# Performance work log

Measured on AMD Instinct MI355X. Metric: run time of the kernel, lower is better.

The kernel has to match this reference:

```python
import jax, jax.numpy as jnp
import numpy as np
from jax import lax

B, T, D, H = 4, 2048, 1024, 8
DK = D // H        # head qk dim (expand_k=1.0) = 128
DV = 2 * D // H    # head v dim (expand_v=2.0) = 256
C = 64             # retention chunk size


def setup_inputs() -> dict:
    key = jax.random.key(0)
    ks = jax.random.split(key, 7)
    s = 0.02
    return {
        "x": jax.random.normal(ks[0], (B, T, D), jnp.float32),
        "Wq": jax.random.normal(ks[1], (D, H * DK), jnp.float32) * s,
        "Wk": jax.random.normal(ks[2], (D, H * DK), jnp.float32) * s,
        "Wv": jax.random.normal(ks[3], (D, H * DV), jnp.float32) * s,
        "Wg": jax.random.normal(ks[4], (D, H * DV), jnp.float32) * s,
        "Wo": jax.random.normal(ks[5], (H * DV, D), jnp.float32) * s,
        "norm_w": jnp.ones((DV,), jnp.float32),
    }


def _rope(x):
    # x: [B,T,H,DK]; GPT-NeoX style (non-interleaved) rotary, base 10000
    half = DK // 2
    inv = 1.0 / (10000.0 ** (jnp.arange(0, DK, 2, dtype=jnp.float32) / DK))
    f = jnp.arange(T, dtype=jnp.float32)[:, None] * inv[None, :]  # [T, half]
    cos = jnp.cos(f)[None, :, None, :]
    sin = jnp.sin(f)[None, :, None, :]
    x1, x2 = x[..., :half], x[..., half:]
    return jnp.concatenate([x1 * cos - x2 * sin, x2 * cos + x1 * sin], axis=-1)


def _retention(q, k, v):
    # chunked decay-gated linear attention (RetNet retention)
    # q,k: [B,T,H,DK], v: [B,T,H,DV]; recurrence S_t = g*S_{t-1} + k_t^T v_t, o_t = q_t S_t
    N = T // C
    gamma = 1.0 - 2.0 ** (-5.0 - jnp.arange(H, dtype=jnp.float32))  # [H] per-head decay
    i = jnp.arange(C, dtype=jnp.float32)
    expo = i[:, None] - i[None, :]                                   # [C,C]
    M = jnp.where(expo >= 0, gamma[:, None, None] ** expo[None], 0.0)  # [H,C,C] intra-chunk decay mask
    dec_q = gamma[:, None] ** (i + 1.0)        # [H,C] decay of state seen by q_i
    dec_k = gamma[:, None] ** (C - 1.0 - i)    # [H,C] decay of k_j into end-of-chunk state
    gC = gamma ** C

    def to_chunks(t):
        return t.reshape(B, N, C, H, -1).transpose(1, 0, 3, 2, 4)  # [N,B,H,C,d]

    qs, kcs, vcs = to_chunks(q), to_chunks(k), to_chunks(v)

    def step(S, inp):
        qc, kc, vc = inp  # [B,H,C,DK],[B,H,C,DK],[B,H,C,DV]
        attn = jnp.einsum('bhid,bhjd->bhij', qc, kc) * M[None]
        o_intra = jnp.einsum('bhij,bhje->bhie', attn, vc)
        o_inter = jnp.einsum('bhid,bhde->bhie', qc, S) * dec_q[None, :, :, None]
        kv = jnp.einsum('bhjd,bhje->bhde', kc * dec_k[None, :, :, None], vc)
        S_new = gC[None, :, None, None] * S + kv
        return S_new, o_intra + o_inter

    S0 = jnp.zeros((B, H, DK, DV), q.dtype)
    _, os_ = lax.scan(step, S0, (qs, kcs, vcs))  # os_: [N,B,H,C,DV]
    return os_.transpose(1, 0, 3, 2, 4).reshape(B, T, H, DV)


def reference(x, Wq, Wk, Wv, Wg, Wo, norm_w):
    q = (x @ Wq).reshape(B, T, H, DK)
    k = (x @ Wk).reshape(B, T, H, DK)
    v = (x @ Wv).reshape(B, T, H, DV)
    g = (x @ Wg).reshape(B, T, H, DV)
    q, k = _rope(q), _rope(k)
    q = q * (DK ** -0.5)
    o = _retention(q, k, v)
    # fused per-head RMSNorm + swish output gate (FusedRMSNormSwishGate)
    rms = jnp.sqrt(jnp.mean(o * o, axis=-1, keepdims=True) + 1e-5)
    o = (o / rms) * norm_w
    o = o * g * jax.nn.sigmoid(g)
    return o.reshape(B, T, H * DV) @ Wo
```

## Files before the change

kernel.cpp:

```cpp
#include <hip/hip_runtime.h>
#include <hip/hip_bf16.h>
#include <cstdint>
#include <cstddef>

using f32x4 = __attribute__((ext_vector_type(4))) float;
using s16x8 = __attribute__((ext_vector_type(8))) short;
using s16x4 = __attribute__((ext_vector_type(4))) short;

#define DEVINL __device__ __forceinline__

static constexpr int T_LEN  = 2048;
static constexpr int MROWS  = 8192;
static constexpr int NCHUNK = 32;

DEVINL float bf2f(short s){
  unsigned u = ((unsigned)(unsigned short)s) << 16;
  return __builtin_bit_cast(float, u);
}
DEVINL short f2bf(float f){
  unsigned u = __builtin_bit_cast(unsigned, f);
  u = (u + 0x7fffu + ((u >> 16) & 1u)) >> 16;
  return (short)(unsigned short)u;
}

#define GLOAD16(gp, lp) \
  __builtin_amdgcn_global_load_lds((__attribute__((address_space(1))) void*)(gp), \
                                   (__attribute__((address_space(3))) void*)(lp), 16, 0, 0)

#define MFMA16(a, b, c) __builtin_amdgcn_mfma_f32_16x16x32_bf16((a), (b), (c), 0, 0, 0)
#define SBAR()  __builtin_amdgcn_sched_barrier(0)
#define WAITVM(n)   asm volatile("s_waitcnt vmcnt(" #n ")" ::: "memory")

__global__ __launch_bounds__(256) void cvt_f32_bf16(const float* __restrict__ in,
                                                    short* __restrict__ out, int n4){
  int i = blockIdx.x * 256 + threadIdx.x;
  if (i >= n4) return;
  float4 v = ((const float4*)in)[i];
  short4 o;
  o.x = f2bf(v.x); o.y = f2bf(v.y); o.z = f2bf(v.z); o.w = f2bf(v.w);
  ((short4*)out)[i] = o;
}

__global__ __launch_bounds__(256) void tr_w(const float* __restrict__ in,
                                            short* __restrict__ out, int R, int C){
  __shared__ float tile[32][33];
  int c0 = blockIdx.x * 32, r0 = blockIdx.y * 32;
  int tx = threadIdx.x, ty = threadIdx.y;
  #pragma unroll
  for (int i = 0; i < 4; ++i){
    int r = ty + i * 8;
    tile[r][tx] = in[(size_t)(r0 + r) * C + c0 + tx];
  }
  __syncthreads();
  #pragma unroll
  for (int i = 0; i < 4; ++i){
    int c = ty + i * 8;
    out[(size_t)(c0 + c) * R + r0 + tx] = f2bf(tile[tx][c]);
  }
}

__global__ __launch_bounds__(256) void tr_w4(const float* __restrict__ Wq,
                                             const float* __restrict__ Wk,
                                             const float* __restrict__ Wv,
                                             const float* __restrict__ Wg,
                                             short* __restrict__ WT){
  __shared__ float tile[32][33];
  int bx = blockIdx.x;
  const float* src; int C; size_t off; int cb;
  if (bx < 32)       { src = Wq; C = 1024; off = 0;                       cb = bx; }
  else if (bx < 64)  { src = Wk; C = 1024; off = (size_t)1024 * 1024;     cb = bx - 32; }
  else if (bx < 128) { src = Wg; C = 2048; off = (size_t)2048 * 1024;     cb = bx - 64; }
  else               { src = Wv; C = 2048; off = (size_t)4096 * 1024;     cb = bx - 128; }
  int c0 = cb * 32, r0 = blockIdx.y * 32;
  int tx = threadIdx.x, ty = threadIdx.y;
  #pragma unroll
  for (int i = 0; i < 4; ++i){
    int r = ty + i * 8;
    tile[r][tx] = src[(size_t)(r0 + r) * C + c0 + tx];
  }
  __syncthreads();
  #pragma unroll
  for (int i = 0; i < 4; ++i){
    int c = ty + i * 8;
    WT[off + (size_t)(c0 + c) * 1024 + r0 + tx] = f2bf(tile[tx][c]);
  }
}

__global__ __launch_bounds__(256) void rope_table(float* __restrict__ tab){
  int i = blockIdx.x * 256 + threadIdx.x;
  int t = i >> 6, d = i & 63;
  float inv = exp2f(-(float)d * (13.287712379549449f / 64.0f));
  float f = (float)t * inv;
  float s, c;
  sincosf(f, &s, &c);
  tab[2 * i]     = c;
  tab[2 * i + 1] = s;
}

__global__ __launch_bounds__(256) void rope_q(short* __restrict__ qb,
                                              const float* __restrict__ tab){
  int idx = blockIdx.x * 256 + threadIdx.x;
  int bt  = idx >> 9, rem = idx & 511;
  int h   = rem >> 6, d = rem & 63;
  int t   = bt & (T_LEN - 1);
  float2 cs = ((const float2*)tab)[t * 64 + d];
  float lg = log2f(1.0f - exp2f(-(float)(5 + h)));
  float mult = 0.08838834764831845f * exp2f((float)((t & 63) + 1) * lg);
  size_t base = (size_t)bt * 1024 + h * 128 + d;
  float x1 = bf2f(qb[base]), x2 = bf2f(qb[base + 64]);
  qb[base]      = f2bf((x1 * cs.x - x2 * cs.y) * mult);
  qb[base + 64] = f2bf((x2 * cs.x + x1 * cs.y) * mult);
}

__global__ __launch_bounds__(256) void rope_k_tr(short* __restrict__ kb,
                                                 short* __restrict__ kTt,
                                                 const float* __restrict__ tab){
  __shared__ alignas(16) short T[64 * 128];
  __shared__ alignas(16) short U[128 * 68];
  const int tid = threadIdx.x, wave = tid >> 6, lane = tid & 63;
  const int bt0 = blockIdx.x * 64, h = blockIdx.y;
  const float lg = log2f(1.0f - exp2f(-(float)(5 + h)));
  #pragma unroll
  for (int c = 0; c < 4; ++c){
    int rbase = c * 16 + wave * 4;
    GLOAD16(kb + (size_t)(bt0 + rbase + (lane >> 4)) * 1024 + h * 128 + (lane & 15) * 8,
            T + rbase * 128);
  }
  WAITVM(0);
  __syncthreads();
  {
    int r = tid >> 2, dbase = (tid & 3) * 16;
    int t = (bt0 + r) & (T_LEN - 1);
    float dec = exp2f((float)(63 - r) * lg);
    s16x8 lo[2], hi[2];
    #pragma unroll
    for (int i = 0; i < 16; ++i){
      int d = dbase + i;
      float2 cs = ((const float2*)tab)[t * 64 + d];
      float x1 = bf2f(T[r * 128 + d]);
      float x2 = bf2f(T[r * 128 + 64 + d]);
      float y1 = x1 * cs.x - x2 * cs.y;
      float y2 = x2 * cs.x + x1 * cs.y;
      lo[i >> 3][i & 7] = f2bf(y1);
      hi[i >> 3][i & 7] = f2bf(y2);
      U[(d)      * 68 + r] = f2bf(y1 * dec);
      U[(d + 64) * 68 + r] = f2bf(y2 * dec);
    }
    size_t gb = (size_t)(bt0 + r) * 1024 + h * 128 + dbase;
    *(s16x8*)&kb[gb]          = lo[0];
    *(s16x8*)&kb[gb + 8]      = lo[1];
    *(s16x8*)&kb[gb + 64]     = hi[0];
    *(s16x8*)&kb[gb + 64 + 8] = hi[1];
  }
  __syncthreads();
  {
    int d = tid >> 1, half = tid & 1;
    const short* src = &U[d * 68 + half * 32];
    size_t gb = (size_t)(h * 128 + d) * MROWS + bt0 + half * 32;
    #pragma unroll
    for (int c = 0; c < 8; ++c)
      *(s16x4*)&kTt[gb + c * 4] = *(const s16x4*)&src[c * 4];
  }
}

DEVINL s16x8 frag64(const short* buf, int row, int ks, int lhi){
  int ch = (ks * 4 + lhi) ^ (row & 7);
  return *(const s16x8*)&buf[row * 64 + ch * 8];
}

template<int MODE>
__global__ __launch_bounds__(512, 2) void gemm256(const short* __restrict__ A,
                                                  const short* __restrict__ Bt,
                                                  void* __restrict__ o0, void* __restrict__ o1,
                                                  void* __restrict__ o2, void* __restrict__ o3,
                                                  int K, int nt, int NT){
  constexpr int BM   = (MODE == 2 ? 128 : 256);
  constexpr int ABUF = BM * 64;
  constexpr int MF   = BM / 32;
  constexpr int MH   = MF / 2;
  __shared__ alignas(16) short LBUF[3 * ABUF + 2 * 16384];
  short* const BB = LBUF + 3 * ABUF;
  const int tid = threadIdx.x, wave = tid >> 6, lane = tid & 63;
  const int l15 = lane & 15, lhi = lane >> 4;
  const int wm = (wave >> 2) * (BM / 2), wn = (wave & 3) * 64;
  const int MG  = (gridDim.x >> 3) / NT;
  const int xcd = blockIdx.x & 7, idx = blockIdx.x >> 3;
  const int mi  = idx % MG, nn = idx / MG;
  const int m0  = (xcd * MG + mi) * BM, n0 = nn * 256;
  const short* Ag = A + (size_t)m0 * K;
  const short* Bg = Bt + (size_t)n0 * K;
  const int sr = lane >> 3;
  const int gc = ((lane & 7) ^ sr) * 8;
  f32x4 acc[MF][4] = {};

  auto stageA = [&](int t, int half){
    short* lb = LBUF + (t % 3) * ABUF;
    size_t k0 = (size_t)t * 64;
    if constexpr (BM == 256){
      #pragma unroll
      for (int c = 0; c < 2; ++c){
        int r0 = half * 128 + c * 64;
        GLOAD16(Ag + (size_t)(r0 + wave * 8 + sr) * K + k0 + gc, lb + (r0 + wave * 8) * 64);
      }
    } else {
      int r0 = half * 64;
      GLOAD16(Ag + (size_t)(r0 + wave * 8 + sr) * K + k0 + gc, lb + (r0 + wave * 8) * 64);
    }
  };
  auto stageB = [&](int t, int half){
    short* lb = BB + (t & 1) * 16384;
    size_t k0 = (size_t)t * 64;
    #pragma unroll
    for (int c = 0; c < 2; ++c){
      int r0 = half * 128 + c * 64;
      GLOAD16(Bg + (size_t)(r0 + wave * 8 + sr) * K + k0 + gc, lb + (r0 + wave * 8) * 64);
    }
  };

  stageA(0, 0); stageA(0, 1); stageB(0, 0); stageB(0, 1);
  stageA(1, 0); stageA(1, 1); stageB(1, 0); stageB(1, 1);
  if constexpr (BM == 256) WAITVM(8); else WAITVM(6);
  __builtin_amdgcn_s_barrier();

  for (int t = 0; t < nt; ++t){
    const short* Ab = LBUF + (t % 3) * ABUF;
    const short* Bb = BB + (t & 1) * 16384;
    s16x8 bfr[2][4];
    s16x8 af[MH][2];
    #pragma unroll
    for (int ks = 0; ks < 2; ++ks)
      #pragma unroll
      for (int nf = 0; nf < 4; ++nf)
        bfr[ks][nf] = frag64(Bb, wn + nf * 16 + l15, ks, lhi);
    #pragma unroll
    for (int i = 0; i < MH; ++i)
      #pragma unroll
      for (int ks = 0; ks < 2; ++ks)
        af[i][ks] = frag64(Ab, wm + i * 16 + l15, ks, lhi);
    if (t + 2 < nt){ stageA(t + 2, 0); stageA(t + 2, 1); }
    __builtin_amdgcn_s_setprio(1);
    #pragma unroll
    for (int ks = 0; ks < 2; ++ks)
      #pragma unroll
      for (int i = 0; i < MH; ++i)
        #pragma unroll
        for (int nf = 0; nf < 4; ++nf){
          if constexpr (MODE == 4)
            acc[i][nf] = MFMA16(af[i][ks], bfr[ks][nf], acc[i][nf]);
          else
            acc[i][nf] = MFMA16(bfr[ks][nf], af[i][ks], acc[i][nf]);
        }
    __builtin_amdgcn_s_setprio(0);
    __builtin_amdgcn_s_barrier();
    if (t + 2 < nt){ stageB(t + 2, 0); stageB(t + 2, 1); }
    #pragma unroll
    for (int i = 0; i < MH; ++i)
      #pragma unroll
      for (int ks = 0; ks < 2; ++ks)
        af[i][ks] = frag64(Ab, wm + (MH + i) * 16 + l15, ks, lhi);
    __builtin_amdgcn_s_setprio(1);
    #pragma unroll
    for (int ks = 0; ks < 2; ++ks)
      #pragma unroll
      for (int i = 0; i < MH; ++i)
        #pragma unroll
        for (int nf = 0; nf < 4; ++nf){
          if constexpr (MODE == 4)
            acc[MH + i][nf] = MFMA16(af[i][ks], bfr[ks][nf], acc[MH + i][nf]);
          else
            acc[MH + i][nf] = MFMA16(bfr[ks][nf], af[i][ks], acc[MH + i][nf]);
        }
    __builtin_amdgcn_s_setprio(0);
    if (t < nt - 2){
      if constexpr (BM == 256) WAITVM(8); else WAITVM(6);
    } else if (t == nt - 2){
      WAITVM(0);
    }
    __builtin_amdgcn_s_barrier();
  }
  if constexpr (MODE == 2){
    float* dst = (float*)o0;
    #pragma unroll
    for (int mf = 0; mf < MF; ++mf){
      int m = m0 + wm + mf * 16 + l15;
      #pragma unroll
      for (int nf = 0; nf < 4; ++nf){
        int nb = n0 + wn + nf * 16 + 4 * lhi;
        *(float4*)&dst[(size_t)m * 1024 + nb] = *(float4*)&acc[mf][nf];
      }
    }
  } else if constexpr (MODE == 4){
    short* dst = (short*)o2;
    #pragma unroll
    for (int mf = 0; mf < MF; ++mf){
      int rb = m0 + wm + mf * 16 + 4 * lhi;
      #pragma unroll
      for (int nf = 0; nf < 4; ++nf){
        int e = n0 + wn + nf * 16 + l15;
        s16x4 pk;
        #pragma unroll
        for (int r = 0; r < 4; ++r) pk[r] = f2bf(acc[mf][nf][r]);
        *(s16x4*)&dst[(size_t)e * MROWS + rb] = pk;
      }
    }
  } else {
    short* dst; int ld, cb;
    if (n0 < 1024)      { dst = (short*)o0; ld = 1024; cb = n0; }
    else if (n0 < 2048) { dst = (short*)o1; ld = 1024; cb = n0 - 1024; }
    else                { dst = (short*)o3; ld = 2048; cb = n0 - 2048; }
    #pragma unroll
    for (int mf = 0; mf < MF; ++mf){
      int m = m0 + wm + mf * 16 + l15;
      #pragma unroll
      for (int nf = 0; nf < 4; ++nf){
        int nb = cb + wn + nf * 16 + 4 * lhi;
        s16x4 pk;
        #pragma unroll
        for (int r = 0; r < 4; ++r) pk[r] = f2bf(acc[mf][nf][r]);
        *(s16x4*)&dst[(size_t)m * ld + nb] = pk;
      }
    }
  }
}

__global__ __launch_bounds__(256) void ret_scan(const short* __restrict__ kT,
                                                const short* __restrict__ vT,
                                                short* __restrict__ ST){
  __shared__ alignas(16) short kbuf[3][4096];
  __shared__ alignas(16) short vbuf[3][4096];
  const int tid = threadIdx.x, wave = tid >> 6, lane = tid & 63;
  const int db = blockIdx.x & 1, eb = blockIdx.x >> 1;
  const int h = blockIdx.y, b = blockIdx.z;
  const int d0 = db * 64, e0 = eb * 64;
  const float lg = log2f(1.0f - exp2f(-(float)(5 + h)));
  const float gC = exp2f(64.0f * lg);
  f32x4 Sacc[4] = {};
  const int srow = wave * 8 + (lane >> 3);
  const int sc   = lane & 7;

  auto STAGE = [&](int n, int buf){
    size_t rowbase = (size_t)(b * T_LEN + n * 64);
    #pragma unroll
    for (int c = 0; c < 2; ++c){
      int r = c * 32 + srow;
      int gc2 = sc ^ (r & 7);
      GLOAD16(kT + (size_t)(h * 128 + d0 + r) * MROWS + rowbase + gc2 * 8,
              &kbuf[buf][c * 2048 + wave * 512]);
    }
    #pragma unroll
    for (int c = 0; c < 2; ++c){
      int r = c * 32 + srow;
      int gc2 = sc ^ (r & 7);
      GLOAD16(vT + (size_t)(h * 256 + e0 + r) * MROWS + rowbase + gc2 * 8,
              &vbuf[buf][c * 2048 + wave * 512]);
    }
  };

  STAGE(0, 0);
  STAGE(1, 1);
  for (int n = 0; n < NCHUNK; ++n){
    const int buf = n % 3;
    if (n + 2 < NCHUNK) STAGE(n + 2, (n + 2) % 3);
    if (n > 0){
      size_t stb = (((size_t)n * 4 + b) * 8 + h) * 32768;
      int dbase = d0 + 16 * wave + 4 * (lane >> 4);
      #pragma unroll
      for (int nf = 0; nf < 4; ++nf){
        int e = e0 + nf * 16 + (lane & 15);
        s16x4 pk;
        #pragma unroll
        for (int r = 0; r < 4; ++r) pk[r] = f2bf(Sacc[nf][r]);
        *(s16x4*)&ST[stb + (size_t)e * 128 + dbase] = pk;
      }
    }
    if (n == 0)       WAITVM(8);
    else if (n < 30)  WAITVM(12);
    else if (n == 30) WAITVM(8);
    else              WAITVM(4);
    __builtin_amdgcn_s_barrier();
    SBAR();
    #pragma unroll
    for (int nf = 0; nf < 4; ++nf)
      #pragma unroll
      for (int r = 0; r < 4; ++r) Sacc[nf][r] *= gC;
    #pragma unroll
    for (int ks = 0; ks < 2; ++ks){
      int d = 16 * wave + (lane & 15);
      int chA = (ks * 4 + (lane >> 4)) ^ (d & 7);
      s16x8 af = *(const s16x8*)&kbuf[buf][d * 64 + chA * 8];
      #pragma unroll
      for (int nf = 0; nf < 4; ++nf){
        int e = nf * 16 + (lane & 15);
        int chB = (ks * 4 + (lane >> 4)) ^ (e & 7);
        s16x8 bv = *(const s16x8*)&vbuf[buf][e * 64 + chB * 8];
        Sacc[nf] = MFMA16(af, bv, Sacc[nf]);
      }
    }
    __builtin_amdgcn_s_barrier();
    SBAR();
  }
}

__global__ __launch_bounds__(256, 2) void ret_fused(const short* __restrict__ q,
                                                    const short* __restrict__ k,
                                                    const short* __restrict__ vT,
                                                    const short* __restrict__ ST,
                                                    const short* __restrict__ g,
                                                    const float* __restrict__ nw,
                                                    short* __restrict__ y){
  __shared__ alignas(16) short GS[16384];
  __shared__ alignas(16) float SS[256];
  __shared__ alignas(16) short XS[16896];
  short* PS = XS;
  short* YT = XS;
  const int tid = threadIdx.x, wave = tid >> 6, lane = tid & 63;
  const int l15 = lane & 15, lhi = lane >> 4;
  const int n = blockIdx.x, h = blockIdx.y, b = blockIdx.z;
  const size_t rowbase = (size_t)(b * T_LEN + n * 64);
  {
    int row = wave * 2 + (lane >> 5), sc32 = lane & 31;
    #pragma unroll
    for (int c = 0; c < 8; ++c){
      int r = c * 8 + row;
      GLOAD16(g + (rowbase + r) * 2048 + h * 256 + sc32 * 8, &GS[c * 2048 + wave * 512]);
    }
  }
  s16x8 Qf[4][4];
  #pragma unroll
  for (int rf = 0; rf < 4; ++rf)
    #pragma unroll
    for (int ks = 0; ks < 4; ++ks)
      Qf[rf][ks] = *(const s16x8*)&q[(rowbase + rf * 16 + l15) * 1024 + h * 128 + ks * 32 + lhi * 8];
  s16x8 Kf[4];
  #pragma unroll
  for (int ks = 0; ks < 4; ++ks)
    Kf[ks] = *(const s16x8*)&k[(rowbase + wave * 16 + l15) * 1024 + h * 128 + ks * 32 + lhi * 8];
  f32x4 accP[4] = {};
  #pragma unroll
  for (int ks = 0; ks < 4; ++ks)
    #pragma unroll
    for (int nf = 0; nf < 4; ++nf)
      accP[nf] = MFMA16(Kf[ks], Qf[nf][ks], accP[nf]);
  const float lg = log2f(1.0f - exp2f(-(float)(5 + h)));
  {
    int jb = wave * 16 + 4 * lhi;
    float dj[4];
    #pragma unroll
    for (int r = 0; r < 4; ++r) dj[r] = exp2f(-(float)(jb + r + 1) * lg);
    #pragma unroll
    for (int nf = 0; nf < 4; ++nf){
      int i = nf * 16 + l15;
      s16x4 pk;
      #pragma unroll
      for (int r = 0; r < 4; ++r)
        pk[r] = f2bf((i >= jb + r) ? accP[nf][r] * dj[r] : 0.0f);
      *(s16x4*)&PS[i * 72 + jb] = pk;
    }
  }
  f32x4 acc[4][4] = {};
  if (n){
    size_t stb = (((size_t)n * 4 + b) * 8 + h) * 32768;
    #pragma unroll
    for (int ks = 0; ks < 4; ++ks){
      s16x8 Sf[4];
      #pragma unroll
      for (int nf = 0; nf < 4; ++nf){
        int e = wave * 64 + nf * 16 + l15;
        Sf[nf] = *(const s16x8*)&ST[stb + (size_t)e * 128 + ks * 32 + lhi * 8];
      }
      #pragma unroll
      for (int mf = 0; mf < 4; ++mf)
        #pragma unroll
        for (int nf = 0; nf < 4; ++nf)
          acc[mf][nf] = MFMA16(Qf[mf][ks], Sf[nf], acc[mf][nf]);
    }
  }
  s16x8 Vf[2][4];
  #pragma unroll
  for (int ks2 = 0; ks2 < 2; ++ks2)
    #pragma unroll
    for (int nf = 0; nf < 4; ++nf){
      int e = wave * 64 + nf * 16 + l15;
      Vf[ks2][nf] = *(const s16x8*)&vT[(size_t)(h * 256 + e) * MROWS + rowbase + ks2 * 32 + lhi * 8];
    }
  __syncthreads();
  #pragma unroll
  for (int ks2 = 0; ks2 < 2; ++ks2){
    s16x8 Pf[4];
    #pragma unroll
    for (int mf = 0; mf < 4; ++mf)
      Pf[mf] = *(const s16x8*)&PS[(mf * 16 + l15) * 72 + ks2 * 32 + lhi * 8];
    #pragma unroll
    for (int mf = 0; mf < 4; ++mf)
      #pragma unroll
      for (int nf = 0; nf < 4; ++nf)
        acc[mf][nf] = MFMA16(Pf[mf], Vf[ks2][nf], acc[mf][nf]);
  }
  float ssp[4][4];
  #pragma unroll
  for (int mf = 0; mf < 4; ++mf)
    #pragma unroll
    for (int r = 0; r < 4; ++r){
      float s = 0.f;
      #pragma unroll
      for (int nf = 0; nf < 4; ++nf) s += acc[mf][nf][r] * acc[mf][nf][r];
      #pragma unroll
      for (int off = 8; off >= 1; off >>= 1) s += __shfl_xor(s, off, 64);
      ssp[mf][r] = s;
    }
  if (l15 == 0){
    #pragma unroll
    for (int mf = 0; mf < 4; ++mf)
      #pragma unroll
      for (int r = 0; r < 4; ++r){
        int row = mf * 16 + 4 * lhi + r;
        SS[row * 4 + wave] = ssp[mf][r];
      }
  }
  __syncthreads();
  #pragma unroll
  for (int mf = 0; mf < 4; ++mf){
    float rr[4];
    #pragma unroll
    for (int r = 0; r < 4; ++r){
      int row = mf * 16 + 4 * lhi + r;
      f32x4 s4 = *(const f32x4*)&SS[row * 4];
      float tot = s4[0] + s4[1] + s4[2] + s4[3];
      rr[r] = __builtin_amdgcn_rsqf(tot * (1.0f / 256.0f) + 1e-5f);
    }
    #pragma unroll
    for (int nf = 0; nf < 4; ++nf){
      int e = wave * 64 + nf * 16 + l15;
      float nwe = nw[e];
      #pragma unroll
      for (int r = 0; r < 4; ++r){
        int row = mf * 16 + 4 * lhi + r;
        float gf = bf2f(GS[row * 256 + e]);
        float sig = __builtin_amdgcn_rcpf(1.0f + exp2f(gf * -1.4426950408889634f));
        YT[row * 264 + e] = f2bf(acc[mf][nf][r] * rr[r] * nwe * gf * sig);
      }
    }
  }
  __syncthreads();
  #pragma unroll
  for (int it = 0; it < 8; ++it){
    int flat = it * 2048 + tid * 8;
    int row = flat >> 8, e = flat & 255;
    s16x8 v = *(const s16x8*)&YT[row * 264 + e];
    *(s16x8*)&y[(rowbase + row) * 2048 + h * 256 + e] = v;
  }
}

extern "C" void kernel_launch(void* const* d_in, const int* in_sizes, int n_in,
                              void* d_out, int out_size, void* d_ws, size_t ws_size,
                              hipStream_t stream){
  const float* x  = (const float*)d_in[0];
  const float* Wq = (const float*)d_in[1];
  const float* Wk = (const float*)d_in[2];
  const float* Wv = (const float*)d_in[3];
  const float* Wg = (const float*)d_in[4];
  const float* Wo = (const float*)d_in[5];
  const float* nw = (const float*)d_in[6];
  float* out = (float*)d_out;

  char* w = (char*)d_ws;
  short* xb  = (short*)w;               w += (size_t)8192 * 1024 * 2;
  short* WT  = (short*)w;               w += (size_t)6144 * 1024 * 2;
  short* kTt = (short*)w;               w += (size_t)1024 * 8192 * 2;
  short* qb  = (short*)w;               w += (size_t)8192 * 1024 * 2;
  short* kb  = (short*)w;               w += (size_t)8192 * 1024 * 2;
  short* vT  = (short*)w;               w += (size_t)2048 * 8192 * 2;
  short* gb  = (short*)w;               w += (size_t)8192 * 2048 * 2;
  short* STb = (short*)w;               w += (size_t)32 * 4 * 8 * 32768 * 2;
  short* WoT = (short*)w;               w += (size_t)1024 * 2048 * 2;
  short* yb  = (short*)d_ws;
  float* tab = (float*)STb;

  cvt_f32_bf16<<<8192, 256, 0, stream>>>(x, xb, 8192 * 1024 / 4);
  dim3 tb(32, 8);
  tr_w4<<<dim3(192, 32), tb, 0, stream>>>(Wq, Wk, Wv, Wg, WT);
  tr_w <<<dim3(32, 64),  tb, 0, stream>>>(Wo, WoT, 2048, 1024);
  rope_table<<<512, 256, 0, stream>>>(tab);

  gemm256<3><<<512, 512, 0, stream>>>(xb, WT, qb, kb, nullptr, gb, 1024, 16, 16);
  gemm256<4><<<256, 512, 0, stream>>>(xb, WT + (size_t)4096 * 1024, nullptr, nullptr, vT, nullptr,
                                      1024, 16, 8);

  rope_q   <<<16384, 256, 0, stream>>>(qb, tab);
  rope_k_tr<<<dim3(128, 8), 256, 0, stream>>>(kb, kTt, tab);

  ret_scan <<<dim3(8, 8, 4),  256, 0, stream>>>(kTt, vT, STb);
  ret_fused<<<dim3(32, 8, 4), 256, 0, stream>>>(qb, kb, vT, STb, gb, nw, yb);

  gemm256<2><<<256, 512, 0, stream>>>(yb, WoT, out, nullptr, nullptr, nullptr, 2048, 32, 4);
}
```

Measured before the change: 280.7 us.

## Replace pipelined output-projection GEMM with simple 128x128 tile kernel

The final Wo projection stops using the 128-row mode of the triple-buffered, software-pipelined gemm256 kernel. It now uses a new, simpler 128x128 tile kernel with 256 threads, a single LDS buffer, syncthreads around each K step, and scalar fp32 stores. This launches 512 blocks instead of 256, which may give better occupancy across CUs. The cost is that global-load latency is no longer overlapped with MFMA work, and the epilogue writes are strided and uncoalesced.

```diff
diff --git a/kernel.cpp b/kernel.cpp
--- a/kernel.cpp
+++ b/kernel.cpp
@@ -174,7 +174,7 @@
                                                   void* __restrict__ o0, void* __restrict__ o1,
                                                   void* __restrict__ o2, void* __restrict__ o3,
                                                   int K, int nt, int NT){
-  constexpr int BM   = (MODE == 2 ? 128 : 256);
+  constexpr int BM   = 256;
   constexpr int ABUF = BM * 64;
   constexpr int MF   = BM / 32;
   constexpr int MH   = MF / 2;
@@ -196,14 +196,9 @@
   auto stageA = [&](int t, int half){
     short* lb = LBUF + (t % 3) * ABUF;
     size_t k0 = (size_t)t * 64;
-    if constexpr (BM == 256){
-      #pragma unroll
-      for (int c = 0; c < 2; ++c){
-        int r0 = half * 128 + c * 64;
-        GLOAD16(Ag + (size_t)(r0 + wave * 8 + sr) * K + k0 + gc, lb + (r0 + wave * 8) * 64);
-      }
-    } else {
-      int r0 = half * 64;
+    #pragma unroll
+    for (int c = 0; c < 2; ++c){
+      int r0 = half * 128 + c * 64;
       GLOAD16(Ag + (size_t)(r0 + wave * 8 + sr) * K + k0 + gc, lb + (r0 + wave * 8) * 64);
     }
   };
@@ -219,7 +214,7 @@
 
   stageA(0, 0); stageA(0, 1); stageB(0, 0); stageB(0, 1);
   stageA(1, 0); stageA(1, 1); stageB(1, 0); stageB(1, 1);
-  if constexpr (BM == 256) WAITVM(8); else WAITVM(6);
+  WAITVM(8);
   __builtin_amdgcn_s_barrier();
 
   for (int t = 0; t < nt; ++t){
@@ -272,24 +267,13 @@
         }
     __builtin_amdgcn_s_setprio(0);
     if (t < nt - 2){
-      if constexpr (BM == 256) WAITVM(8); else WAITVM(6);
+      WAITVM(8);
     } else if (t == nt - 2){
       WAITVM(0);
     }
     __builtin_amdgcn_s_barrier();
   }
-  if constexpr (MODE == 2){
-    float* dst = (float*)o0;
-    #pragma unroll
-    for (int mf = 0; mf < MF; ++mf){
-      int m = m0 + wm + mf * 16 + l15;
-      #pragma unroll
-      for (int nf = 0; nf < 4; ++nf){
-        int nb = n0 + wn + nf * 16 + 4 * lhi;
-        *(float4*)&dst[(size_t)m * 1024 + nb] = *(float4*)&acc[mf][nf];
-      }
-    }
-  } else if constexpr (MODE == 4){
+  if constexpr (MODE == 4){
     short* dst = (short*)o2;
     #pragma unroll
     for (int mf = 0; mf < MF; ++mf){
@@ -319,6 +303,64 @@
         for (int r = 0; r < 4; ++r) pk[r] = f2bf(acc[mf][nf][r]);
         *(s16x4*)&dst[(size_t)m * ld + nb] = pk;
       }
+    }
+  }
+}
+
+__global__ __launch_bounds__(256) void gemm_bt_f32(const short* __restrict__ A,
+                                                   const short* __restrict__ Bt,
+                                                   float* __restrict__ out, int K, int N){
+  __shared__ alignas(16) short As[128 * 64];
+  __shared__ alignas(16) short Bs[128 * 64];
+  const int tid = threadIdx.x, wave = tid >> 6, lane = tid & 63;
+  const int m0 = blockIdx.x * 128, n0 = blockIdx.y * 128;
+  const int wm = (wave & 1) * 64, wn = (wave >> 1) * 64;
+  f32x4 acc[4][4] = {};
+  const int srow = wave * 8 + (lane >> 3);
+  const int sc   = lane & 7;
+  const int kT = K >> 6;
+  for (int kt = 0; kt < kT; ++kt){
+    const int k0 = kt << 6;
+    #pragma unroll
+    for (int c = 0; c < 4; ++c){
+      int row = c * 32 + srow;
+      int gc  = sc ^ (row & 7);
+      GLOAD16(A  + (size_t)(m0 + row) * K + k0 + gc * 8, &As[c * 2048 + wave * 512]);
+      GLOAD16(Bt + (size_t)(n0 + row) * K + k0 + gc * 8, &Bs[c * 2048 + wave * 512]);
+    }
+    __syncthreads();
+    #pragma unroll
+    for (int ks = 0; ks < 2; ++ks){
+      s16x8 af[4], bfr[4];
+      #pragma unroll
+      for (int mf = 0; mf < 4; ++mf){
+        int row = wm + mf * 16 + (lane & 15);
+        int ch  = (ks * 4 + (lane >> 4)) ^ (row & 7);
+        af[mf] = *(const s16x8*)&As[row * 64 + ch * 8];
+      }
+      #pragma unroll
+      for (int nf = 0; nf < 4; ++nf){
+        int row = wn + nf * 16 + (lane & 15);
+        int ch  = (ks * 4 + (lane >> 4)) ^ (row & 7);
+        bfr[nf] = *(const s16x8*)&Bs[row * 64 + ch * 8];
+      }
+      #pragma unroll
+      for (int mf = 0; mf < 4; ++mf)
+        #pragma unroll
+        for (int nf = 0; nf < 4; ++nf)
+          acc[mf][nf] = MFMA16(af[mf], bfr[nf], acc[mf][nf]);
+    }
+    __syncthreads();
+  }
+  #pragma unroll
+  for (int mf = 0; mf < 4; ++mf){
+    #pragma unroll
+    for (int nf = 0; nf < 4; ++nf){
+      int col   = n0 + wn + nf * 16 + (lane & 15);
+      int rbase = m0 + wm + mf * 16 + 4 * (lane >> 4);
+      f32x4 v = acc[mf][nf];
+      #pragma unroll
+      for (int r = 0; r < 4; ++r) out[(size_t)(rbase + r) * N + col] = v[r];
     }
   }
 }
@@ -592,5 +634,5 @@
   ret_scan <<<dim3(8, 8, 4),  256, 0, stream>>>(kTt, vT, STb);
   ret_fused<<<dim3(32, 8, 4), 256, 0, stream>>>(qb, kb, vT, STb, gb, nw, yb);
 
-  gemm256<2><<<256, 512, 0, stream>>>(yb, WoT, out, nullptr, nullptr, nullptr, 2048, 32, 4);
-}
+  gemm_bt_f32<<<dim3(64, 8), 256, 0, stream>>>(yb, WoT, out, 2048, 1024);
+}
```

Measured after the change: 285.7 us. About the same (+1.8%).
